# Optimization experiments

Measured on AMD Instinct MI355X. Metric: run time of the kernel, lower is better.

Reference implementation:

```python
import jax, jax.numpy as jnp
import numpy as np

N_NODES = 100000
LAYER_NUM = 3


def gcn_conv(x, src, dst, W, b, n):
    # PyG GCNConv: add self-loops, symmetric normalization D^-1/2 (A+I) D^-1/2, x@W, +b
    h = x @ W                                   # [N, out]
    ones = jnp.ones(src.shape[0], dtype=h.dtype)
    deg = jax.ops.segment_sum(ones, dst, num_segments=n) + 1.0  # +1 for self-loop
    dinv = jax.lax.rsqrt(deg)                   # deg >= 1 always (self-loop)
    norm = dinv[src] * dinv[dst]                # [E]
    msgs = h[src] * norm[:, None]               # gather + scale, [E, out]
    agg = jax.ops.segment_sum(msgs, dst, num_segments=n)
    agg = agg + h * (dinv * dinv)[:, None]      # self-loop contribution
    return agg + b


def setup_inputs() -> dict:
    key = jax.random.key(0)
    ks = jax.random.split(key, 8)
    in_d, mid_d, out_d = 512, 256, 40
    n, e = N_NODES, 1600000
    x = jax.random.normal(ks[0], (n, in_d), dtype=jnp.float32)
    edge_index = jax.random.randint(ks[1], (2, e), 0, n, dtype=jnp.int64)
    def glorot(k, fan_in, fan_out):
        s = jnp.sqrt(6.0 / (fan_in + fan_out))
        return jax.random.uniform(k, (fan_in, fan_out), jnp.float32, -s, s)
    W1 = glorot(ks[2], in_d, mid_d)
    b1 = jnp.zeros((mid_d,), jnp.float32)
    Wi = glorot(ks[3], mid_d, mid_d)
    bi = jnp.zeros((mid_d,), jnp.float32)
    W2 = glorot(ks[4], mid_d, out_d)
    b2 = jnp.zeros((out_d,), jnp.float32)
    return {"x": x, "edge_index": edge_index, "W1": W1, "b1": b1,
            "Wi": Wi, "bi": bi, "W2": W2, "b2": b2}


def reference(x, edge_index, W1, b1, Wi, bi, W2, b2):
    n = x.shape[0]
    src, dst = edge_index[0], edge_index[1]
    h = gcn_conv(x, src, dst, W1, b1, n)
    for _ in range(LAYER_NUM):
        h = gcn_conv(h, src, dst, Wi, bi, n)
        h = jax.nn.relu(h)
    emb = h  # detached embedding in original
    h = jax.nn.relu(h)
    h = gcn_conv(h, src, dst, W2, b2, n)
    return (jax.nn.log_softmax(h, axis=1), emb)
```

## Files before the change

### kernel.cpp

```cpp
#include <hip/hip_runtime.h>
#include <cmath>

typedef __attribute__((ext_vector_type(8))) short short8v;
typedef __attribute__((ext_vector_type(4))) short short4v;
typedef __attribute__((ext_vector_type(4))) float f32x4;

__device__ inline short f2bf(float f) {
  union { float f; unsigned u; } a; a.f = f;
  unsigned r = a.u + 0x7FFF + ((a.u >> 16) & 1);
  return (short)(r >> 16);
}
__device__ inline float bf2f(short b) {
  union { unsigned u; float f; } a; a.u = ((unsigned)(unsigned short)b) << 16;
  return a.f;
}

__global__ __launch_bounds__(256) void bin_edges2_kernel(
    const int* __restrict__ src, const int* __restrict__ dst,
    int* __restrict__ bktCur, uint2* __restrict__ pairBuf,
    int e, int cap, int nbk) {
  __shared__ int hist[512];
  __shared__ int lbase[512];
  __shared__ int cur[512];
  int t = threadIdx.x;
  for (int i = t; i < nbk; i += 256) hist[i] = 0;
  __syncthreads();
  int chunk = (e + gridDim.x - 1) / gridDim.x;
  int s0 = blockIdx.x * chunk;
  int s1 = s0 + chunk; if (s1 > e) s1 = e;
  for (int j = s0 + t; j < s1; j += 256)
    atomicAdd(&hist[((unsigned)dst[j]) >> 8], 1);
  __syncthreads();
  for (int i = t; i < nbk; i += 256) {
    int c = hist[i];
    lbase[i] = c ? atomicAdd(&bktCur[i], c) : 0;
    cur[i] = 0;
  }
  __syncthreads();
  for (int j = s0 + t; j < s1; j += 256) {
    int d = dst[j], s = src[j];
    int b = ((unsigned)d) >> 8;
    int q = atomicAdd(&cur[b], 1);
    pairBuf[(size_t)b * cap + lbase[b] + q] = make_uint2((unsigned)d, (unsigned)s);
  }
}

__global__ void scan_bkt_kernel(const int* __restrict__ bktCur, int* __restrict__ bktOff,
                                int nb) {
  __shared__ int s[512];
  int t = threadIdx.x;
  int v = (t < nb) ? bktCur[t] : 0;
  s[t] = v;
  for (int off = 1; off < 512; off <<= 1) {
    __syncthreads();
    int add = (t >= off) ? s[t - off] : 0;
    __syncthreads();
    s[t] += add;
  }
  if (t < nb) bktOff[t] = s[t] - v;
}

__global__ __launch_bounds__(256) void bucket_csr_kernel(
    const uint2* __restrict__ pairBuf, const int* __restrict__ bktCur,
    const int* __restrict__ bktOff, int* __restrict__ deg, int* __restrict__ rs,
    float* __restrict__ dinv, int* __restrict__ col, int n, int cap) {
  __shared__ int hist[256];
  __shared__ int loff[256];
  __shared__ int cur[256];
  int b = blockIdx.x;
  int base = b << 8;
  int m = n - base; if (m > 256) m = 256;
  int t = threadIdx.x;
  hist[t] = 0;
  __syncthreads();
  int cnt = bktCur[b];
  const uint2* pb = pairBuf + (size_t)b * cap;
  for (int j = t; j < cnt; j += 256)
    atomicAdd(&hist[pb[j].x - base], 1);
  __syncthreads();
  int own = hist[t];
  loff[t] = own;
  for (int off = 1; off < 256; off <<= 1) {
    __syncthreads();
    int add = (t >= off) ? loff[t - off] : 0;
    __syncthreads();
    loff[t] += add;
  }
  __syncthreads();
  int excl = loff[t] - own;
  int bo = bktOff[b];
  if (t < m) {
    deg[base + t] = own;
    rs[base + t] = bo + excl;
    dinv[base + t] = rsqrtf((float)own + 1.0f);
  }
  __syncthreads();
  hist[t] = excl;
  cur[t] = 0;
  __syncthreads();
  for (int j = t; j < cnt; j += 256) {
    int d = pb[j].x - base;
    int q = atomicAdd(&cur[d], 1);
    col[bo + hist[d] + q] = (int)pb[j].y;
  }
}

__global__ void convert_wt_kernel(const float* __restrict__ W, short* __restrict__ Wt,
                                  int K, int N) {
  int i = blockIdx.x * blockDim.x + threadIdx.x;
  if (i < K * N) {
    int k = i / N, nn = i - k * N;
    Wt[nn * K + k] = f2bf(W[i]);
  }
}

__global__ void convert_w2t_kernel(const float* __restrict__ W2, short* __restrict__ W2t) {
  int i = blockIdx.x * blockDim.x + threadIdx.x;
  if (i < 64 * 256) {
    int c = i >> 8, k = i & 255;
    W2t[i] = (c < 40) ? f2bf(W2[k * 40 + c]) : (short)0;
  }
}

template <int K, bool AF32>
__global__ __launch_bounds__(256, 2) void gemm_mfma_kernel(
    const void* __restrict__ Aptr, const short* __restrict__ Wt,
    const float* __restrict__ dinv, char* __restrict__ G8,
    float* __restrict__ gscale, int n) {
  __shared__ short As[64 * 64];
  __shared__ short Bs[256 * 64];
  __shared__ float rmax[4][64];
  int tid = threadIdx.x;
  int lane = tid & 63, wn = tid >> 6;
  int l15 = lane & 15, lh = lane >> 4;
  int rowBase = blockIdx.x * 64;

  f32x4 acc[4][4];
#pragma unroll
  for (int mi = 0; mi < 4; mi++)
#pragma unroll
    for (int ni = 0; ni < 4; ni++) acc[mi][ni] = (f32x4){0.f, 0.f, 0.f, 0.f};

  short8v aS[2], bS[8];

  auto LOAD = [&](int kt) {
#pragma unroll
    for (int i = 0; i < 2; i++) {
      int s = tid + i * 256;
      int r = s >> 3, u = s & 7;
      int gr = rowBase + r; if (gr >= n) gr = n - 1;
      if constexpr (AF32) {
        const float* ap = (const float*)Aptr + (size_t)gr * K + kt + u * 8;
        float4 f0 = *(const float4*)ap;
        float4 f1 = *(const float4*)(ap + 4);
        short8v v;
        v[0] = f2bf(f0.x); v[1] = f2bf(f0.y); v[2] = f2bf(f0.z); v[3] = f2bf(f0.w);
        v[4] = f2bf(f1.x); v[5] = f2bf(f1.y); v[6] = f2bf(f1.z); v[7] = f2bf(f1.w);
        aS[i] = v;
      } else {
        aS[i] = *(const short8v*)((const short*)Aptr + (size_t)gr * K + kt + u * 8);
      }
    }
#pragma unroll
    for (int i = 0; i < 8; i++) {
      int s = tid + i * 256;
      int r = s >> 3, u = s & 7;
      bS[i] = *(const short8v*)(Wt + (size_t)r * K + kt + u * 8);
    }
  };

  auto STORE = [&]() {
#pragma unroll
    for (int i = 0; i < 2; i++) {
      int s = tid + i * 256;
      int r = s >> 3, u = s & 7;
      *(short8v*)&As[r * 64 + ((u ^ (r & 7)) << 3)] = aS[i];
    }
#pragma unroll
    for (int i = 0; i < 8; i++) {
      int s = tid + i * 256;
      int r = s >> 3, u = s & 7;
      *(short8v*)&Bs[r * 64 + ((u ^ (r & 7)) << 3)] = bS[i];
    }
  };

  auto COMPUTE = [&]() {
#pragma unroll
    for (int kk = 0; kk < 2; kk++) {
      int u = kk * 4 + lh;
      short8v af[4], bf[4];
#pragma unroll
      for (int mi = 0; mi < 4; mi++) {
        int r = mi * 16 + l15;
        af[mi] = *(const short8v*)&As[r * 64 + ((u ^ (r & 7)) << 3)];
      }
#pragma unroll
      for (int ni = 0; ni < 4; ni++) {
        int r = wn * 64 + ni * 16 + l15;
        bf[ni] = *(const short8v*)&Bs[r * 64 + ((u ^ (r & 7)) << 3)];
      }
#pragma unroll
      for (int mi = 0; mi < 4; mi++)
#pragma unroll
        for (int ni = 0; ni < 4; ni++)
          acc[mi][ni] = __builtin_amdgcn_mfma_f32_16x16x32_bf16(
              af[mi], bf[ni], acc[mi][ni], 0, 0, 0);
    }
  };

  LOAD(0);
  STORE();
  __syncthreads();
  for (int kt = 64; kt < K; kt += 64) {
    LOAD(kt);
    COMPUTE();
    __syncthreads();
    STORE();
    __syncthreads();
  }
  COMPUTE();

#pragma unroll
  for (int mi = 0; mi < 4; mi++) {
#pragma unroll
    for (int j = 0; j < 4; j++) {
      float mx = 0.f;
#pragma unroll
      for (int ni = 0; ni < 4; ni++) mx = fmaxf(mx, fabsf(acc[mi][ni][j]));
      for (int off = 1; off < 16; off <<= 1)
        mx = fmaxf(mx, __shfl_xor(mx, off, 64));
      if (l15 == 0) rmax[wn][mi * 16 + lh * 4 + j] = mx;
    }
  }
  __syncthreads();
#pragma unroll
  for (int mi = 0; mi < 4; mi++) {
#pragma unroll
    for (int j = 0; j < 4; j++) {
      int r = mi * 16 + lh * 4 + j;
      int gr = rowBase + r;
      if (gr < n) {
        float cmax = fmaxf(fmaxf(rmax[0][r], rmax[1][r]),
                           fmaxf(rmax[2][r], rmax[3][r]));
        float inv = (cmax > 0.f) ? 127.f / cmax : 0.f;
        if (wn == 0 && l15 == 0)
          gscale[gr] = dinv[gr] * cmax * (1.f / 127.f);
#pragma unroll
        for (int ni = 0; ni < 4; ni++) {
          int gc = wn * 64 + ni * 16 + l15;
          int q = (int)rintf(acc[mi][ni][j] * inv);
          G8[(size_t)gr * 256 + gc] = (char)q;
        }
      }
    }
  }
}

__global__ __launch_bounds__(256, 3) void gemm_mfma40_kernel(
    const short* __restrict__ Hb, const short* __restrict__ W2t,
    const float* __restrict__ dinv, short* __restrict__ G2b, int n) {
  __shared__ short As[256 * 64];
  __shared__ short Bs[64 * 64];
  int tid = threadIdx.x;
  int lane = tid & 63, wid = tid >> 6;
  int l15 = lane & 15, lh = lane >> 4;
  int rowBase = blockIdx.x * 256;

  f32x4 acc[4][4];
#pragma unroll
  for (int mi = 0; mi < 4; mi++)
#pragma unroll
    for (int ni = 0; ni < 4; ni++) acc[mi][ni] = (f32x4){0.f, 0.f, 0.f, 0.f};

  for (int kt = 0; kt < 256; kt += 64) {
#pragma unroll
    for (int i = 0; i < 8; i++) {
      int s = tid + i * 256;
      int r = s >> 3, u = s & 7;
      int gr = rowBase + r; if (gr >= n) gr = n - 1;
      short8v v = *(const short8v*)(Hb + (size_t)gr * 256 + kt + u * 8);
      *(short8v*)&As[r * 64 + ((u ^ (r & 7)) << 3)] = v;
    }
#pragma unroll
    for (int i = 0; i < 2; i++) {
      int s = tid + i * 256;
      int r = s >> 3, u = s & 7;
      short8v v = *(const short8v*)(W2t + (size_t)r * 256 + kt + u * 8);
      *(short8v*)&Bs[r * 64 + ((u ^ (r & 7)) << 3)] = v;
    }
    __syncthreads();
#pragma unroll
    for (int kk = 0; kk < 2; kk++) {
      int u = kk * 4 + lh;
      short8v af[4], bf[4];
#pragma unroll
      for (int mi = 0; mi < 4; mi++) {
        int r = wid * 64 + mi * 16 + l15;
        af[mi] = *(const short8v*)&As[r * 64 + ((u ^ (r & 7)) << 3)];
      }
#pragma unroll
      for (int ni = 0; ni < 4; ni++) {
        int r = ni * 16 + l15;
        bf[ni] = *(const short8v*)&Bs[r * 64 + ((u ^ (r & 7)) << 3)];
      }
#pragma unroll
      for (int mi = 0; mi < 4; mi++)
#pragma unroll
        for (int ni = 0; ni < 4; ni++)
          acc[mi][ni] = __builtin_amdgcn_mfma_f32_16x16x32_bf16(
              af[mi], bf[ni], acc[mi][ni], 0, 0, 0);
    }
    __syncthreads();
  }

#pragma unroll
  for (int mi = 0; mi < 4; mi++) {
#pragma unroll
    for (int j = 0; j < 4; j++) {
      int gr = rowBase + wid * 64 + mi * 16 + lh * 4 + j;
      if (gr < n) {
        float sc = dinv[gr];
#pragma unroll
        for (int ni = 0; ni < 4; ni++) {
          int gc = ni * 16 + l15;
          if (gc < 40) G2b[(size_t)gr * 40 + gc] = f2bf(acc[mi][ni][j] * sc);
        }
      }
    }
  }
}

__device__ inline void dq_acc(int w, float s, float& a0, float& a1,
                              float& a2, float& a3) {
  a0 += (float)(signed char)(w & 0xff) * s;
  a1 += (float)(signed char)((w >> 8) & 0xff) * s;
  a2 += (float)(signed char)((w >> 16) & 0xff) * s;
  a3 += (float)(signed char)(w >> 24) * s;
}

template <int RELU, int WF32>
__global__ __launch_bounds__(256) void aggregate_i8_kernel(
    const char* __restrict__ G8, const float* __restrict__ gsc,
    const int* __restrict__ col, const int* __restrict__ rs,
    const int* __restrict__ deg, const float* __restrict__ dinv,
    const float* __restrict__ bias, short* __restrict__ Hb,
    float* __restrict__ Hf, int n) {
  int wid = threadIdx.x >> 6;
  int lane = threadIdx.x & 63;
  int v = blockIdx.x * 4 + wid;
  if (v >= n) return;
  float a0 = 0.f, a1 = 0.f, a2 = 0.f, a3 = 0.f;
  {
    int w = *(const int*)(G8 + (size_t)v * 256 + lane * 4);
    dq_acc(w, gsc[v], a0, a1, a2, a3);
  }
  int base = rs[v], cnt = deg[v];
  for (int i0 = 0; i0 < cnt; i0 += 64) {
    int rem = cnt - i0; if (rem > 64) rem = 64;
    int ci = col[base + i0 + (lane < rem ? lane : 0)];
    int i = 0;
    for (; i + 8 <= rem; i += 8) {
      int u0 = __shfl(ci, i + 0), u1 = __shfl(ci, i + 1);
      int u2 = __shfl(ci, i + 2), u3 = __shfl(ci, i + 3);
      int u4 = __shfl(ci, i + 4), u5 = __shfl(ci, i + 5);
      int u6 = __shfl(ci, i + 6), u7 = __shfl(ci, i + 7);
      int w0 = *(const int*)(G8 + (size_t)u0 * 256 + lane * 4);
      int w1 = *(const int*)(G8 + (size_t)u1 * 256 + lane * 4);
      int w2 = *(const int*)(G8 + (size_t)u2 * 256 + lane * 4);
      int w3 = *(const int*)(G8 + (size_t)u3 * 256 + lane * 4);
      int w4 = *(const int*)(G8 + (size_t)u4 * 256 + lane * 4);
      int w5 = *(const int*)(G8 + (size_t)u5 * 256 + lane * 4);
      int w6 = *(const int*)(G8 + (size_t)u6 * 256 + lane * 4);
      int w7 = *(const int*)(G8 + (size_t)u7 * 256 + lane * 4);
      float s0 = gsc[u0], s1 = gsc[u1], s2 = gsc[u2], s3 = gsc[u3];
      float s4 = gsc[u4], s5 = gsc[u5], s6 = gsc[u6], s7 = gsc[u7];
      dq_acc(w0, s0, a0, a1, a2, a3);
      dq_acc(w1, s1, a0, a1, a2, a3);
      dq_acc(w2, s2, a0, a1, a2, a3);
      dq_acc(w3, s3, a0, a1, a2, a3);
      dq_acc(w4, s4, a0, a1, a2, a3);
      dq_acc(w5, s5, a0, a1, a2, a3);
      dq_acc(w6, s6, a0, a1, a2, a3);
      dq_acc(w7, s7, a0, a1, a2, a3);
    }
    for (; i < rem; i++) {
      int u = __shfl(ci, i);
      int w = *(const int*)(G8 + (size_t)u * 256 + lane * 4);
      dq_acc(w, gsc[u], a0, a1, a2, a3);
    }
  }
  float s = dinv[v];
  float4 b4 = ((const float4*)bias)[lane];
  float o0 = a0 * s + b4.x, o1 = a1 * s + b4.y, o2 = a2 * s + b4.z, o3 = a3 * s + b4.w;
  if (RELU) {
    o0 = fmaxf(o0, 0.f); o1 = fmaxf(o1, 0.f);
    o2 = fmaxf(o2, 0.f); o3 = fmaxf(o3, 0.f);
  }
  short4v ob; ob[0] = f2bf(o0); ob[1] = f2bf(o1); ob[2] = f2bf(o2); ob[3] = f2bf(o3);
  *(short4v*)(Hb + (size_t)v * 256 + lane * 4) = ob;
  if (WF32) {
    float4 of; of.x = o0; of.y = o1; of.z = o2; of.w = o3;
    *(float4*)(Hf + (size_t)v * 256 + lane * 4) = of;
  }
}

__global__ __launch_bounds__(256) void agg40_lsm_kernel(
    const short* __restrict__ G2b, const int* __restrict__ col,
    const int* __restrict__ rs, const int* __restrict__ deg,
    const float* __restrict__ dinv, const float* __restrict__ b2,
    float* __restrict__ out, int n) {
  int wid = threadIdx.x >> 6;
  int lane = threadIdx.x & 63;
  int v = blockIdx.x * 4 + wid;
  if (v >= n) return;
  bool act = lane < 40;
  int ln = act ? lane : 0;
  float acc = act ? bf2f(G2b[(size_t)v * 40 + lane]) : 0.f;
  int base = rs[v], cnt = deg[v];
  for (int i0 = 0; i0 < cnt; i0 += 64) {
    int rem = cnt - i0; if (rem > 64) rem = 64;
    int ci = col[base + i0 + (lane < rem ? lane : 0)];
    int i = 0;
    for (; i + 4 <= rem; i += 4) {
      int u0 = __shfl(ci, i + 0), u1 = __shfl(ci, i + 1);
      int u2 = __shfl(ci, i + 2), u3 = __shfl(ci, i + 3);
      float x0 = bf2f(G2b[(size_t)u0 * 40 + ln]);
      float x1 = bf2f(G2b[(size_t)u1 * 40 + ln]);
      float x2 = bf2f(G2b[(size_t)u2 * 40 + ln]);
      float x3 = bf2f(G2b[(size_t)u3 * 40 + ln]);
      acc += x0 + x1 + x2 + x3;
    }
    for (; i < rem; i++) {
      int u = __shfl(ci, i);
      acc += bf2f(G2b[(size_t)u * 40 + ln]);
    }
  }
  float val;
  if (act) val = acc * dinv[v] + b2[lane];
  else val = -INFINITY;
  float m = val;
  for (int off = 32; off; off >>= 1) m = fmaxf(m, __shfl_xor(m, off, 64));
  float e = act ? expf(val - m) : 0.f;
  float ssum = e;
  for (int off = 32; off; off >>= 1) ssum += __shfl_xor(ssum, off, 64);
  if (act) out[(size_t)v * 40 + lane] = val - m - logf(ssum);
}


static inline size_t alignup(size_t x) { return (x + 255) & ~(size_t)255; }

extern "C" void kernel_launch(void* const* d_in, const int* in_sizes, int n_in,
                              void* d_out, int out_size, void* d_ws, size_t ws_size,
                              hipStream_t stream) {
  const float* x  = (const float*)d_in[0];
  const int*   ei = (const int*)d_in[1];
  const float* W1 = (const float*)d_in[2];
  const float* b1 = (const float*)d_in[3];
  const float* Wi = (const float*)d_in[4];
  const float* bi = (const float*)d_in[5];
  const float* W2 = (const float*)d_in[6];
  const float* b2 = (const float*)d_in[7];

  const int in_d = 512, mid_d = 256, out_d = 40;
  int n = in_sizes[0] / in_d;
  int E = in_sizes[1] / 2;
  const int* src = ei;
  const int* dst = ei + E;

  float* out_lsm = (float*)d_out;
  float* emb     = (float*)d_out + (size_t)n * out_d;

  int NB = (n + 255) >> 8;
  int cap = ((E / NB) * 3) / 2 + 1024;

  char* w = (char*)d_ws;
  float* dinv  = (float*)w;  w += alignup((size_t)n * 4);
  int* deg     = (int*)w;    w += alignup((size_t)n * 4);
  int* rs      = (int*)w;    w += alignup((size_t)n * 4);
  int* colidx  = (int*)w;    w += alignup((size_t)E * 4);
  int* bktCur  = (int*)w;    w += alignup((size_t)NB * 4);
  int* bktOff  = (int*)w;    w += alignup((size_t)NB * 4);
  uint2* pairBuf = (uint2*)w; w += alignup((size_t)NB * cap * 8);
  short* W1t   = (short*)w;  w += alignup((size_t)mid_d * in_d * 2);
  short* Wit   = (short*)w;  w += alignup((size_t)mid_d * mid_d * 2);
  short* W2t   = (short*)w;  w += alignup((size_t)64 * mid_d * 2);
  char* G8     = (char*)w;   w += alignup((size_t)n * mid_d);
  float* gsc   = (float*)w;  w += alignup((size_t)n * 4);
  short* Hb    = (short*)w;  w += alignup((size_t)n * mid_d * 2);
  short* G2b   = (short*)G8;

  hipMemsetAsync(bktCur, 0, (size_t)NB * 4, stream);
  bin_edges2_kernel<<<256, 256, 0, stream>>>(src, dst, bktCur, pairBuf, E, cap, NB);
  scan_bkt_kernel<<<1, 512, 0, stream>>>(bktCur, bktOff, NB);
  bucket_csr_kernel<<<NB, 256, 0, stream>>>(pairBuf, bktCur, bktOff,
                                            deg, rs, dinv, colidx, n, cap);

  convert_wt_kernel<<<(in_d * mid_d + 255) / 256, 256, 0, stream>>>(W1, W1t, in_d, mid_d);
  convert_wt_kernel<<<(mid_d * mid_d + 255) / 256, 256, 0, stream>>>(Wi, Wit, mid_d, mid_d);
  convert_w2t_kernel<<<(64 * mid_d + 255) / 256, 256, 0, stream>>>(W2, W2t);

  int ggrid = (n + 63) / 64;
  int agg_grid = (n + 3) / 4;

  gemm_mfma_kernel<512, true><<<ggrid, 256, 0, stream>>>(x, W1t, dinv, G8, gsc, n);
  aggregate_i8_kernel<0, 0><<<agg_grid, 256, 0, stream>>>(
      G8, gsc, colidx, rs, deg, dinv, b1, Hb, nullptr, n);
  for (int l = 0; l < 2; l++) {
    gemm_mfma_kernel<256, false><<<ggrid, 256, 0, stream>>>(Hb, Wit, dinv, G8, gsc, n);
    aggregate_i8_kernel<1, 0><<<agg_grid, 256, 0, stream>>>(
        G8, gsc, colidx, rs, deg, dinv, bi, Hb, nullptr, n);
  }
  gemm_mfma_kernel<256, false><<<ggrid, 256, 0, stream>>>(Hb, Wit, dinv, G8, gsc, n);
  aggregate_i8_kernel<1, 1><<<agg_grid, 256, 0, stream>>>(
      G8, gsc, colidx, rs, deg, dinv, bi, Hb, emb, n);

  gemm_mfma40_kernel<<<(n + 255) / 256, 256, 0, stream>>>(Hb, W2t, dinv, G2b, n);
  agg40_lsm_kernel<<<agg_grid, 256, 0, stream>>>(G2b, colidx, rs, deg, dinv, b2, out_lsm, n);
}
```

Measured before the change: 671.2 us.

## Load GEMM tiles directly into LDS via global_load_lds, drop register prefetch

Replaces the register-staged global→LDS copies in both MFMA GEMM kernels with the direct global-to-LDS load builtin, keeping the XOR swizzle by permuting the source addresses per lane. This removes the register double-buffer and the explicit LDS store instructions, which lowers VGPR pressure. It also drops the software prefetch overlap, so each k-tile now waits for its load before compute. The 40-column GEMM's launch bound changes from 3 to 2 blocks per CU.

```diff
diff --git a/kernel.cpp b/kernel.cpp
--- a/kernel.cpp
+++ b/kernel.cpp
@@ -13,6 +13,12 @@
 __device__ inline float bf2f(short b) {
   union { unsigned u; float f; } a; a.u = ((unsigned)(unsigned short)b) << 16;
   return a.f;
+}
+
+__device__ inline void gload16(const void* g, void* l) {
+  __builtin_amdgcn_global_load_lds(
+      (const __attribute__((address_space(1))) void*)g,
+      (__attribute__((address_space(3))) void*)l, 16, 0, 0);
 }
 
 __global__ __launch_bounds__(256) void bin_edges2_kernel(
@@ -133,6 +139,7 @@
   int tid = threadIdx.x;
   int lane = tid & 63, wn = tid >> 6;
   int l15 = lane & 15, lh = lane >> 4;
+  int lr = lane >> 3, lu = lane & 7;
   int rowBase = blockIdx.x * 64;
 
   f32x4 acc[4][4];
@@ -141,50 +148,38 @@
 #pragma unroll
     for (int ni = 0; ni < 4; ni++) acc[mi][ni] = (f32x4){0.f, 0.f, 0.f, 0.f};
 
-  short8v aS[2], bS[8];
-
-  auto LOAD = [&](int kt) {
-#pragma unroll
-    for (int i = 0; i < 2; i++) {
-      int s = tid + i * 256;
-      int r = s >> 3, u = s & 7;
-      int gr = rowBase + r; if (gr >= n) gr = n - 1;
-      if constexpr (AF32) {
+  for (int kt = 0; kt < K; kt += 64) {
+#pragma unroll
+    for (int c = 0; c < 8; c++) {
+      int r = wn * 64 + c * 8 + lr;
+      int up = lu ^ (r & 7);
+      gload16(Wt + (size_t)r * K + kt + up * 8, &Bs[(wn * 64 + c * 8) * 64]);
+    }
+    if constexpr (AF32) {
+#pragma unroll
+      for (int i = 0; i < 2; i++) {
+        int s = tid + i * 256;
+        int r = s >> 3, u = s & 7;
+        int gr = rowBase + r; if (gr >= n) gr = n - 1;
         const float* ap = (const float*)Aptr + (size_t)gr * K + kt + u * 8;
         float4 f0 = *(const float4*)ap;
         float4 f1 = *(const float4*)(ap + 4);
         short8v v;
         v[0] = f2bf(f0.x); v[1] = f2bf(f0.y); v[2] = f2bf(f0.z); v[3] = f2bf(f0.w);
         v[4] = f2bf(f1.x); v[5] = f2bf(f1.y); v[6] = f2bf(f1.z); v[7] = f2bf(f1.w);
-        aS[i] = v;
-      } else {
-        aS[i] = *(const short8v*)((const short*)Aptr + (size_t)gr * K + kt + u * 8);
-      }
-    }
-#pragma unroll
-    for (int i = 0; i < 8; i++) {
-      int s = tid + i * 256;
-      int r = s >> 3, u = s & 7;
-      bS[i] = *(const short8v*)(Wt + (size_t)r * K + kt + u * 8);
-    }
-  };
-
-  auto STORE = [&]() {
-#pragma unroll
-    for (int i = 0; i < 2; i++) {
-      int s = tid + i * 256;
-      int r = s >> 3, u = s & 7;
-      *(short8v*)&As[r * 64 + ((u ^ (r & 7)) << 3)] = aS[i];
-    }
-#pragma unroll
-    for (int i = 0; i < 8; i++) {
-      int s = tid + i * 256;
-      int r = s >> 3, u = s & 7;
-      *(short8v*)&Bs[r * 64 + ((u ^ (r & 7)) << 3)] = bS[i];
-    }
-  };
-
-  auto COMPUTE = [&]() {
+        *(short8v*)&As[r * 64 + ((u ^ (r & 7)) << 3)] = v;
+      }
+    } else {
+#pragma unroll
+      for (int c = 0; c < 2; c++) {
+        int r = wn * 16 + c * 8 + lr;
+        int gr = rowBase + r; if (gr >= n) gr = n - 1;
+        int up = lu ^ (r & 7);
+        gload16((const short*)Aptr + (size_t)gr * K + kt + up * 8,
+                &As[(wn * 16 + c * 8) * 64]);
+      }
+    }
+    __syncthreads();
 #pragma unroll
     for (int kk = 0; kk < 2; kk++) {
       int u = kk * 4 + lh;
@@ -206,19 +201,8 @@
           acc[mi][ni] = __builtin_amdgcn_mfma_f32_16x16x32_bf16(
               af[mi], bf[ni], acc[mi][ni], 0, 0, 0);
     }
-  };
-
-  LOAD(0);
-  STORE();
-  __syncthreads();
-  for (int kt = 64; kt < K; kt += 64) {
-    LOAD(kt);
-    COMPUTE();
-    __syncthreads();
-    STORE();
-    __syncthreads();
-  }
-  COMPUTE();
+    __syncthreads();
+  }
 
 #pragma unroll
   for (int mi = 0; mi < 4; mi++) {
@@ -256,7 +240,7 @@
   }
 }
 
-__global__ __launch_bounds__(256, 3) void gemm_mfma40_kernel(
+__global__ __launch_bounds__(256, 2) void gemm_mfma40_kernel(
     const short* __restrict__ Hb, const short* __restrict__ W2t,
     const float* __restrict__ dinv, short* __restrict__ G2b, int n) {
   __shared__ short As[256 * 64];
@@ -264,6 +248,7 @@
   int tid = threadIdx.x;
   int lane = tid & 63, wid = tid >> 6;
   int l15 = lane & 15, lh = lane >> 4;
+  int lr = lane >> 3, lu = lane & 7;
   int rowBase = blockIdx.x * 256;
 
   f32x4 acc[4][4];
@@ -274,19 +259,17 @@
 
   for (int kt = 0; kt < 256; kt += 64) {
 #pragma unroll
-    for (int i = 0; i < 8; i++) {
-      int s = tid + i * 256;
-      int r = s >> 3, u = s & 7;
+    for (int c = 0; c < 8; c++) {
+      int r = wid * 64 + c * 8 + lr;
       int gr = rowBase + r; if (gr >= n) gr = n - 1;
-      short8v v = *(const short8v*)(Hb + (size_t)gr * 256 + kt + u * 8);
-      *(short8v*)&As[r * 64 + ((u ^ (r & 7)) << 3)] = v;
-    }
-#pragma unroll
-    for (int i = 0; i < 2; i++) {
-      int s = tid + i * 256;
-      int r = s >> 3, u = s & 7;
-      short8v v = *(const short8v*)(W2t + (size_t)r * 256 + kt + u * 8);
-      *(short8v*)&Bs[r * 64 + ((u ^ (r & 7)) << 3)] = v;
+      int up = lu ^ (r & 7);
+      gload16(Hb + (size_t)gr * 256 + kt + up * 8, &As[(wid * 64 + c * 8) * 64]);
+    }
+#pragma unroll
+    for (int c = 0; c < 2; c++) {
+      int r = wid * 16 + c * 8 + lr;
+      int up = lu ^ (r & 7);
+      gload16(W2t + (size_t)r * 256 + kt + up * 8, &Bs[(wid * 16 + c * 8) * 64]);
     }
     __syncthreads();
 #pragma unroll
```

New measurement: 681.2 us. No clear change (+1.5%).
